# Kernel tuning notes

Measured on AMD Instinct MI355X. Metric: run time of the kernel, lower is better.

The kernel has to match this reference:

```python
import jax, jax.numpy as jnp
import numpy as np

N = 100000
E = 1600000
D_IN = 256
HID = 128
EPS = 1e-5


def setup_inputs() -> dict:
    key = jax.random.key(0)
    ks = jax.random.split(key, 8)
    x = jax.random.normal(ks[0], (N, D_IN), dtype=jnp.float32)
    edge_index = jax.random.randint(ks[1], (2, E), 0, N, dtype=jnp.int64)
    edge_weight = jax.random.uniform(ks[2], (E,), dtype=jnp.float32)
    # GCNConv lin weights (glorot-ish scale) + bias
    W1 = jax.random.normal(ks[3], (D_IN, HID), dtype=jnp.float32) / np.sqrt(D_IN)
    b1 = jnp.zeros((HID,), dtype=jnp.float32)
    W2 = jax.random.normal(ks[4], (HID, HID), dtype=jnp.float32) / np.sqrt(HID)
    b2 = jnp.zeros((HID,), dtype=jnp.float32)
    # BatchNorm affine params
    g1 = jnp.ones((HID,), dtype=jnp.float32)
    be1 = jnp.zeros((HID,), dtype=jnp.float32)
    g2 = jnp.ones((HID,), dtype=jnp.float32)
    be2 = jnp.zeros((HID,), dtype=jnp.float32)
    return {"x": x, "edge_index": edge_index, "edge_weight": edge_weight,
            "W1": W1, "b1": b1, "g1": g1, "be1": be1,
            "W2": W2, "b2": b2, "g2": g2, "be2": be2}


def _gcn_layer(h, src, dst, w, W, b):
    # GCNConv(add_self_loops=False, normalize=False):
    # h' = h @ W; out[i] = sum_{(j->i)} w_ji * h'[j]; out += b
    h = h @ W                                   # [N, out_dim]
    msg = w[:, None] * jnp.take(h, src, axis=0)  # [E, out_dim]
    agg = jax.ops.segment_sum(msg, dst, num_segments=N)
    return agg + b


def _bn(h, gamma, beta):
    # BatchNorm1d with batch statistics (biased variance), training-mode math
    mean = jnp.mean(h, axis=0)
    var = jnp.mean(jnp.square(h - mean), axis=0)
    return (h - mean) * jax.lax.rsqrt(var + EPS) * gamma + beta


def reference(x, edge_index, edge_weight, W1, b1, g1, be1, W2, b2, g2, be2):
    src = edge_index[0]
    dst = edge_index[1]
    h = _gcn_layer(x, src, dst, edge_weight, W1, b1)
    h = jax.nn.relu(_bn(h, g1, be1))
    h = _gcn_layer(h, src, dst, edge_weight, W2, b2)
    h = jax.nn.relu(_bn(h, g2, be2))  # last_activation=True
    return h
```

## Files before the change

### kernel.cpp

```cpp
#include <hip/hip_runtime.h>
#include <hip/hip_bf16.h>

#define NNODES 100000
#define DIN    256
#define NHID   128
#define EPS    1e-5f
#define SHIFT  9
#define NB2    ((NNODES + 511) >> SHIFT)
#define BCAP2  9216
#define CURPAD 16
#define PH     2048

typedef __attribute__((ext_vector_type(8))) short short8v;
typedef __attribute__((ext_vector_type(4))) float f32x4;

static __device__ __forceinline__ unsigned short f2bf(float v) {
    __hip_bfloat16 b = __float2bfloat16(v);
    return *reinterpret_cast<unsigned short*>(&b);
}
static __device__ __forceinline__ float bfhi2f(unsigned int u) {
    union { unsigned int i; float f; } x; x.i = u & 0xFFFF0000u; return x.f;
}
static __device__ __forceinline__ float bflo2f(unsigned int u) {
    union { unsigned int i; float f; } x; x.i = u << 16; return x.f;
}

__global__ __launch_bounds__(256) void prep_kernel(const float* __restrict__ W1,
                                                   const float* __restrict__ W2,
                                                   unsigned short* __restrict__ Wt1,
                                                   unsigned short* __restrict__ Wt2,
                                                   int* __restrict__ gcur,
                                                   float* __restrict__ sums) {
    int i = blockIdx.x * 256 + threadIdx.x;
    if (i < DIN * NHID) {
        const int k = i >> 7, c = i & 127;
        Wt1[c * DIN + k] = f2bf(W1[i]);
        return;
    }
    i -= DIN * NHID;
    if (i < NHID * NHID) {
        const int k = i >> 7, c = i & 127;
        Wt2[c * NHID + k] = f2bf(W2[i]);
        return;
    }
    i -= NHID * NHID;
    if (i < NB2 * CURPAD) { gcur[i] = 0; return; }
    i -= NB2 * CURPAD;
    if (i < 512) sums[i] = 0.f;
}

template <int K, int MODE>
__global__ __launch_bounds__(256) void mfma_gemm(const float* __restrict__ Af,
                                                 const unsigned short* __restrict__ Wtb,
                                                 const float* __restrict__ SS,
                                                 unsigned short* __restrict__ C, int M) {
    constexpr int NS = K / 32;
    constexpr int PADB = 40;
    __shared__ unsigned short As[2][64 * PADB];
    __shared__ float ssl[256];

    const int t = threadIdx.x;
    if (MODE == 1) {
        ssl[t] = SS[t];
        __syncthreads();
    }

    const int wid = t >> 6;
    const int lane = t & 63;
    const int wr = wid >> 1, wc = wid & 1;
    const int l15 = lane & 15, g = lane >> 4;
    const int R0 = blockIdx.x * 64;
    const int RW = R0 + wr * 32;

    const int srow = t >> 2;
    const int scol = (t & 3) * 8;

    f32x4 acc[2][4] = {};

    auto STAGE = [&](int s, int buf) {
        const int k0 = s * 32;
        int grow = R0 + srow;
        grow = grow < M ? grow : M - 1;
        const float* p = Af + (size_t)grow * K + k0 + scol;
        float4 v0 = *reinterpret_cast<const float4*>(p);
        float4 v1 = *reinterpret_cast<const float4*>(p + 4);
        if (MODE == 1) {
            const int c0 = k0 + scol;
            v0.x = fmaxf(fmaf(v0.x, ssl[c0],     ssl[128 + c0]),     0.f);
            v0.y = fmaxf(fmaf(v0.y, ssl[c0 + 1], ssl[128 + c0 + 1]), 0.f);
            v0.z = fmaxf(fmaf(v0.z, ssl[c0 + 2], ssl[128 + c0 + 2]), 0.f);
            v0.w = fmaxf(fmaf(v0.w, ssl[c0 + 3], ssl[128 + c0 + 3]), 0.f);
            v1.x = fmaxf(fmaf(v1.x, ssl[c0 + 4], ssl[128 + c0 + 4]), 0.f);
            v1.y = fmaxf(fmaf(v1.y, ssl[c0 + 5], ssl[128 + c0 + 5]), 0.f);
            v1.z = fmaxf(fmaf(v1.z, ssl[c0 + 6], ssl[128 + c0 + 6]), 0.f);
            v1.w = fmaxf(fmaf(v1.w, ssl[c0 + 7], ssl[128 + c0 + 7]), 0.f);
        }
        unsigned short bv[8];
        bv[0] = f2bf(v0.x); bv[1] = f2bf(v0.y); bv[2] = f2bf(v0.z); bv[3] = f2bf(v0.w);
        bv[4] = f2bf(v1.x); bv[5] = f2bf(v1.y); bv[6] = f2bf(v1.z); bv[7] = f2bf(v1.w);
        *reinterpret_cast<uint4*>(&As[buf][srow * PADB + scol]) =
            *reinterpret_cast<const uint4*>(bv);
    };

    STAGE(0, 0);
    __syncthreads();

    for (int s = 0; s < NS; ++s) {
        if (s + 1 < NS) STAGE(s + 1, (s + 1) & 1);
        const unsigned short* ab = As[s & 1];
        short8v b[4];
#pragma unroll
        for (int n = 0; n < 4; ++n) {
            const int col = wc * 64 + n * 16 + l15;
            b[n] = *reinterpret_cast<const short8v*>(&Wtb[(size_t)col * K + s * 32 + g * 8]);
        }
        short8v a[2];
#pragma unroll
        for (int m = 0; m < 2; ++m) {
            const int row = wr * 32 + m * 16 + l15;
            a[m] = *reinterpret_cast<const short8v*>(&ab[row * PADB + g * 8]);
        }
#pragma unroll
        for (int m = 0; m < 2; ++m)
#pragma unroll
            for (int n = 0; n < 4; ++n)
                acc[m][n] = __builtin_amdgcn_mfma_f32_16x16x32_bf16(a[m], b[n], acc[m][n], 0, 0, 0);
        __syncthreads();
    }

#pragma unroll
    for (int m = 0; m < 2; ++m) {
#pragma unroll
        for (int q = 0; q < 4; ++q) {
            const int row = RW + m * 16 + g * 4 + q;
            if (row < M) {
                unsigned short* cp = C + (size_t)row * NHID + wc * 64 + l15;
#pragma unroll
                for (int n = 0; n < 4; ++n)
                    cp[n * 16] = f2bf(acc[m][n][q]);
            }
        }
    }
}

__global__ __launch_bounds__(256) void part_kernel(const int* __restrict__ src,
                                                   const int* __restrict__ dst,
                                                   const float* __restrict__ w,
                                                   int* __restrict__ gcur,
                                                   int2* __restrict__ bstage, int E) {
    __shared__ int2 staged[PH];
    __shared__ unsigned char aux[PH];
    __shared__ int hist[NB2], scn[NB2], cur[NB2], gbase[NB2];
    __shared__ int part[256];

    const int t = threadIdx.x;
    const int nchunk = (E + PH - 1) / PH;
    for (int c = blockIdx.x; c < nchunk; c += gridDim.x) {
        const int e0 = c * PH;
        const int cnt = min(PH, E - e0);
        for (int i = t; i < NB2; i += 256) hist[i] = 0;
        __syncthreads();

        int2 pay[8];
        int bk[8];
#pragma unroll
        for (int j = 0; j < 8; ++j) {
            const int i = j * 256 + t;
            bk[j] = -1;
            if (i < cnt) {
                const int e = e0 + i;
                const int d = dst[e];
                bk[j] = d >> SHIFT;
                pay[j].x = src[e] | ((d & 511) << 17);
                pay[j].y = __float_as_int(w[e]);
                atomicAdd(&hist[bk[j]], 1);
            }
        }
        __syncthreads();

        part[t] = (t < NB2) ? hist[t] : 0;
        __syncthreads();
        for (int off = 1; off < 256; off <<= 1) {
            const int v = (t >= off) ? part[t - off] : 0;
            __syncthreads();
            part[t] += v;
            __syncthreads();
        }
        if (t < NB2) {
            const int ex = part[t] - hist[t];
            scn[t] = ex;
            cur[t] = ex;
        }
        __syncthreads();

#pragma unroll
        for (int j = 0; j < 8; ++j) {
            if (bk[j] >= 0) {
                const int p = atomicAdd(&cur[bk[j]], 1);
                staged[p] = pay[j];
                aux[p] = (unsigned char)bk[j];
            }
        }
        if (t < NB2 && hist[t] > 0) gbase[t] = atomicAdd(&gcur[t * CURPAD], hist[t]);
        __syncthreads();

        for (int i = t; i < cnt; i += 256) {
            const int b = aux[i];
            const int p = gbase[b] + (i - scn[b]);
            if (p < BCAP2) bstage[(size_t)b * BCAP2 + p] = staged[i];
        }
        __syncthreads();
    }
}

__global__ __launch_bounds__(512) void csr_kernel(const int* __restrict__ gcur,
                                                  const int2* __restrict__ bstage,
                                                  int2* __restrict__ row_be,
                                                  int2* __restrict__ s_iw) {
    const int b = blockIdx.x;
    const int t = threadIdx.x;
    int cnt = gcur[b * CURPAD];
    if (cnt > BCAP2) cnt = BCAP2;
    const int sbase = b * BCAP2;

    __shared__ int hist[512], cur[512];
    __shared__ int part[512];
    hist[t] = 0;
    __syncthreads();
    for (int i = t; i < cnt; i += 512)
        atomicAdd(&hist[(bstage[sbase + i].x >> 17) & 511], 1);
    __syncthreads();

    part[t] = hist[t];
    __syncthreads();
    for (int off = 1; off < 512; off <<= 1) {
        const int v = (t >= off) ? part[t - off] : 0;
        __syncthreads();
        part[t] += v;
        __syncthreads();
    }
    const int excl = part[t] - hist[t];
    cur[t] = excl;
    const int d = (b << SHIFT) + t;
    if (d < NNODES) {
        int2 be;
        be.x = sbase + excl;
        be.y = sbase + part[t];
        row_be[d] = be;
    }
    __syncthreads();

    for (int i = t; i < cnt; i += 512) {
        const int2 e = bstage[sbase + i];
        const int l = (e.x >> 17) & 511;
        const int p = atomicAdd(&cur[l], 1);
        int2 o;
        o.x = e.x & 0x1FFFF;
        o.y = e.y;
        s_iw[sbase + p] = o;
    }
}

__global__ __launch_bounds__(256) void aggregate_kernel(const unsigned short* __restrict__ hb,
                                                        const int2* __restrict__ row_be,
                                                        const int2* __restrict__ s_iw,
                                                        float* __restrict__ out, int n) {
    const int wid = (blockIdx.x * 256 + threadIdx.x) >> 6;
    if (wid >= n) return;
    const int lane = threadIdx.x & 63;
    const int grp = lane >> 4;
    const int l16 = lane & 15;
    const int2 be = row_be[wid];
    const int end = be.y;

    float acc[8] = {};
    int j = be.x + grp;
    for (; j + 4 < end; j += 8) {
        const int2 e0 = s_iw[j];
        const int2 e1 = s_iw[j + 4];
        const uint4 v0 = *reinterpret_cast<const uint4*>(hb + (size_t)e0.x * NHID + l16 * 8);
        const uint4 v1 = *reinterpret_cast<const uint4*>(hb + (size_t)e1.x * NHID + l16 * 8);
        const float w0 = __int_as_float(e0.y);
        const float w1 = __int_as_float(e1.y);
        acc[0] = fmaf(w0, bflo2f(v0.x), acc[0]); acc[1] = fmaf(w0, bfhi2f(v0.x), acc[1]);
        acc[2] = fmaf(w0, bflo2f(v0.y), acc[2]); acc[3] = fmaf(w0, bfhi2f(v0.y), acc[3]);
        acc[4] = fmaf(w0, bflo2f(v0.z), acc[4]); acc[5] = fmaf(w0, bfhi2f(v0.z), acc[5]);
        acc[6] = fmaf(w0, bflo2f(v0.w), acc[6]); acc[7] = fmaf(w0, bfhi2f(v0.w), acc[7]);
        acc[0] = fmaf(w1, bflo2f(v1.x), acc[0]); acc[1] = fmaf(w1, bfhi2f(v1.x), acc[1]);
        acc[2] = fmaf(w1, bflo2f(v1.y), acc[2]); acc[3] = fmaf(w1, bfhi2f(v1.y), acc[3]);
        acc[4] = fmaf(w1, bflo2f(v1.z), acc[4]); acc[5] = fmaf(w1, bfhi2f(v1.z), acc[5]);
        acc[6] = fmaf(w1, bflo2f(v1.w), acc[6]); acc[7] = fmaf(w1, bfhi2f(v1.w), acc[7]);
    }
    if (j < end) {
        const int2 e0 = s_iw[j];
        const uint4 v0 = *reinterpret_cast<const uint4*>(hb + (size_t)e0.x * NHID + l16 * 8);
        const float w0 = __int_as_float(e0.y);
        acc[0] = fmaf(w0, bflo2f(v0.x), acc[0]); acc[1] = fmaf(w0, bfhi2f(v0.x), acc[1]);
        acc[2] = fmaf(w0, bflo2f(v0.y), acc[2]); acc[3] = fmaf(w0, bfhi2f(v0.y), acc[3]);
        acc[4] = fmaf(w0, bflo2f(v0.z), acc[4]); acc[5] = fmaf(w0, bfhi2f(v0.z), acc[5]);
        acc[6] = fmaf(w0, bflo2f(v0.w), acc[6]); acc[7] = fmaf(w0, bfhi2f(v0.w), acc[7]);
    }
#pragma unroll
    for (int k = 0; k < 8; ++k) {
        acc[k] += __shfl_xor(acc[k], 16, 64);
        acc[k] += __shfl_xor(acc[k], 32, 64);
    }
    if (grp == 0) {
        float4 a, b;
        a.x = acc[0]; a.y = acc[1]; a.z = acc[2]; a.w = acc[3];
        b.x = acc[4]; b.y = acc[5]; b.z = acc[6]; b.w = acc[7];
        float4* op = reinterpret_cast<float4*>(out + (size_t)wid * NHID + l16 * 8);
        op[0] = a;
        op[1] = b;
    }
}

__global__ __launch_bounds__(256) void stats_kernel(const float* __restrict__ h,
                                                    float* __restrict__ sums, int nrows) {
    const int col = threadIdx.x & 127;
    const int half = threadIdx.x >> 7;
    float s = 0.f, sq = 0.f;
    for (int r = blockIdx.x * 2 + half; r < nrows; r += gridDim.x * 2) {
        const float v = h[(size_t)r * NHID + col];
        s += v;
        sq += v * v;
    }
    __shared__ float ls[256], lq[256];
    ls[threadIdx.x] = s;
    lq[threadIdx.x] = sq;
    __syncthreads();
    if (threadIdx.x < 128) {
        atomicAdd(&sums[col], ls[threadIdx.x] + ls[threadIdx.x + 128]);
        atomicAdd(&sums[128 + col], lq[threadIdx.x] + lq[threadIdx.x + 128]);
    }
}

__global__ void finalize_kernel(const float* __restrict__ sums,
                                const float* __restrict__ gamma,
                                const float* __restrict__ beta,
                                float* __restrict__ ss) {
    const int c = threadIdx.x;
    const float invN = 1.0f / (float)NNODES;
    const float mean = sums[c] * invN;
    const float var = sums[128 + c] * invN - mean * mean;
    const float scale = gamma[c] * rsqrtf(var + EPS);
    ss[c] = scale;
    ss[128 + c] = beta[c] - mean * scale;
}

__global__ __launch_bounds__(256) void apply_f32_kernel(const float* __restrict__ in,
                                                        const float* __restrict__ ss,
                                                        float* __restrict__ out, int n4) {
    const int idx = blockIdx.x * 256 + threadIdx.x;
    if (idx >= n4) return;
    const int c = (idx & 31) * 4;
    const float4 v = reinterpret_cast<const float4*>(in)[idx];
    const float4 sc = *reinterpret_cast<const float4*>(ss + c);
    const float4 sh = *reinterpret_cast<const float4*>(ss + 128 + c);
    float4 r;
    r.x = fmaxf(fmaf(v.x, sc.x, sh.x), 0.f);
    r.y = fmaxf(fmaf(v.y, sc.y, sh.y), 0.f);
    r.z = fmaxf(fmaf(v.z, sc.z, sh.z), 0.f);
    r.w = fmaxf(fmaf(v.w, sc.w, sh.w), 0.f);
    reinterpret_cast<float4*>(out)[idx] = r;
}

extern "C" void kernel_launch(void* const* d_in, const int* in_sizes, int n_in,
                              void* d_out, int out_size, void* d_ws, size_t ws_size,
                              hipStream_t stream) {
    const float* x   = (const float*)d_in[0];
    const int*   ei  = (const int*)d_in[1];
    const float* ew  = (const float*)d_in[2];
    const float* W1  = (const float*)d_in[3];
    const float* g1  = (const float*)d_in[5];
    const float* be1 = (const float*)d_in[6];
    const float* W2  = (const float*)d_in[7];
    const float* g2  = (const float*)d_in[9];
    const float* be2 = (const float*)d_in[10];
    float* out = (float*)d_out;

    const int M = NNODES;
    const int E = in_sizes[2];
    const int* src = ei;
    const int* dst = ei + E;

    unsigned short* hb = (unsigned short*)d_ws;
    float* agg   = (float*)(hb + (size_t)M * NHID);
    int2* bstage = (int2*)(agg + (size_t)M * NHID);
    int2* s_iw   = bstage + (size_t)NB2 * BCAP2;
    int2* row_be = s_iw + (size_t)NB2 * BCAP2;
    int* gcur    = (int*)(row_be + NNODES);
    unsigned short* Wt1b = (unsigned short*)(gcur + NB2 * CURPAD);
    unsigned short* Wt2b = Wt1b + DIN * NHID;
    float* sums  = (float*)(Wt2b + NHID * NHID);
    float* ss    = sums + 512;

    const int gemm_grid = (M + 63) / 64;
    const int n4 = M * NHID / 4;
    const int app_grid = (n4 + 255) / 256;
    const int agg_grid = (M * 64 + 255) / 256;
    const int part_grid = (E + PH - 1) / PH;
    const int prep_tot = DIN * NHID + NHID * NHID + NB2 * CURPAD + 512;

    prep_kernel<<<(prep_tot + 255) / 256, 256, 0, stream>>>(W1, W2, Wt1b, Wt2b, gcur, sums);
    part_kernel<<<part_grid, 256, 0, stream>>>(src, dst, ew, gcur, bstage, E);
    csr_kernel<<<NB2, 512, 0, stream>>>(gcur, bstage, row_be, s_iw);

    mfma_gemm<DIN, 0><<<gemm_grid, 256, 0, stream>>>(x, Wt1b, nullptr, hb, M);
    aggregate_kernel<<<agg_grid, 256, 0, stream>>>(hb, row_be, s_iw, agg, M);
    stats_kernel<<<1024, 256, 0, stream>>>(agg, sums, M);
    finalize_kernel<<<1, 128, 0, stream>>>(sums, g1, be1, ss);

    mfma_gemm<NHID, 1><<<gemm_grid, 256, 0, stream>>>(agg, Wt2b, ss, hb, M);
    aggregate_kernel<<<agg_grid, 256, 0, stream>>>(hb, row_be, s_iw, agg, M);
    stats_kernel<<<1024, 256, 0, stream>>>(agg, sums + 256, M);
    finalize_kernel<<<1, 128, 0, stream>>>(sums + 256, g2, be2, ss);
    apply_f32_kernel<<<app_grid, 256, 0, stream>>>(agg, ss, out, n4);
}
```

Before: 336.6 us.

## Fuse GEMM1 with edge partition, store aggregates in bf16, fold BN finalize

```diff
diff --git a/kernel.cpp b/kernel.cpp
--- a/kernel.cpp
+++ b/kernel.cpp
@@ -49,116 +49,96 @@
     if (i < 512) sums[i] = 0.f;
 }
 
-template <int K, int MODE>
-__global__ __launch_bounds__(256) void mfma_gemm(const float* __restrict__ Af,
-                                                 const unsigned short* __restrict__ Wtb,
-                                                 const float* __restrict__ SS,
-                                                 unsigned short* __restrict__ C, int M) {
-    constexpr int NS = K / 32;
-    constexpr int PADB = 40;
-    __shared__ unsigned short As[2][64 * PADB];
-    __shared__ float ssl[256];
+__global__ __launch_bounds__(256) void gemm1_part_kernel(
+    const float* __restrict__ Af, const unsigned short* __restrict__ Wtb,
+    unsigned short* __restrict__ C, int M, int ngemm,
+    const int* __restrict__ src, const int* __restrict__ dst,
+    const float* __restrict__ w, int* __restrict__ gcur,
+    int2* __restrict__ bstage, int E) {
+    struct GemmS { unsigned short As[2][64 * 40]; };
+    struct PartS {
+        int2 staged[PH];
+        int hist[NB2], scn[NB2], cur[NB2], gbase[NB2];
+        int pscan[256];
+        unsigned char aux[PH];
+    };
+    __shared__ union { GemmS g; PartS p; } sm;
 
     const int t = threadIdx.x;
-    if (MODE == 1) {
-        ssl[t] = SS[t];
-        __syncthreads();
-    }
-
-    const int wid = t >> 6;
-    const int lane = t & 63;
-    const int wr = wid >> 1, wc = wid & 1;
-    const int l15 = lane & 15, g = lane >> 4;
-    const int R0 = blockIdx.x * 64;
-    const int RW = R0 + wr * 32;
-
-    const int srow = t >> 2;
-    const int scol = (t & 3) * 8;
-
-    f32x4 acc[2][4] = {};
-
-    auto STAGE = [&](int s, int buf) {
-        const int k0 = s * 32;
-        int grow = R0 + srow;
-        grow = grow < M ? grow : M - 1;
-        const float* p = Af + (size_t)grow * K + k0 + scol;
-        float4 v0 = *reinterpret_cast<const float4*>(p);
-        float4 v1 = *reinterpret_cast<const float4*>(p + 4);
-        if (MODE == 1) {
-            const int c0 = k0 + scol;
-            v0.x = fmaxf(fmaf(v0.x, ssl[c0],     ssl[128 + c0]),     0.f);
-            v0.y = fmaxf(fmaf(v0.y, ssl[c0 + 1], ssl[128 + c0 + 1]), 0.f);
-            v0.z = fmaxf(fmaf(v0.z, ssl[c0 + 2], ssl[128 + c0 + 2]), 0.f);
-            v0.w = fmaxf(fmaf(v0.w, ssl[c0 + 3], ssl[128 + c0 + 3]), 0.f);
-            v1.x = fmaxf(fmaf(v1.x, ssl[c0 + 4], ssl[128 + c0 + 4]), 0.f);
-            v1.y = fmaxf(fmaf(v1.y, ssl[c0 + 5], ssl[128 + c0 + 5]), 0.f);
-            v1.z = fmaxf(fmaf(v1.z, ssl[c0 + 6], ssl[128 + c0 + 6]), 0.f);
-            v1.w = fmaxf(fmaf(v1.w, ssl[c0 + 7], ssl[128 + c0 + 7]), 0.f);
-        }
-        unsigned short bv[8];
-        bv[0] = f2bf(v0.x); bv[1] = f2bf(v0.y); bv[2] = f2bf(v0.z); bv[3] = f2bf(v0.w);
-        bv[4] = f2bf(v1.x); bv[5] = f2bf(v1.y); bv[6] = f2bf(v1.z); bv[7] = f2bf(v1.w);
-        *reinterpret_cast<uint4*>(&As[buf][srow * PADB + scol]) =
-            *reinterpret_cast<const uint4*>(bv);
-    };
-
-    STAGE(0, 0);
-    __syncthreads();
-
-    for (int s = 0; s < NS; ++s) {
-        if (s + 1 < NS) STAGE(s + 1, (s + 1) & 1);
-        const unsigned short* ab = As[s & 1];
-        short8v b[4];
-#pragma unroll
-        for (int n = 0; n < 4; ++n) {
-            const int col = wc * 64 + n * 16 + l15;
-            b[n] = *reinterpret_cast<const short8v*>(&Wtb[(size_t)col * K + s * 32 + g * 8]);
-        }
-        short8v a[2];
+    if (blockIdx.x < ngemm) {
+        constexpr int K = DIN;
+        constexpr int NS = K / 32;
+        constexpr int PADB = 40;
+        const int wid = t >> 6;
+        const int lane = t & 63;
+        const int wr = wid >> 1, wc = wid & 1;
+        const int l15 = lane & 15, g = lane >> 4;
+        const int R0 = blockIdx.x * 64;
+        const int RW = R0 + wr * 32;
+        const int srow = t >> 2;
+        const int scol = (t & 3) * 8;
+
+        f32x4 acc[2][4] = {};
+
+        auto STAGE = [&](int s, int buf) {
+            const int k0 = s * 32;
+            int grow = R0 + srow;
+            grow = grow < M ? grow : M - 1;
+            const float* p = Af + (size_t)grow * K + k0 + scol;
+            const float4 v0 = *reinterpret_cast<const float4*>(p);
+            const float4 v1 = *reinterpret_cast<const float4*>(p + 4);
+            unsigned short bv[8];
+            bv[0] = f2bf(v0.x); bv[1] = f2bf(v0.y); bv[2] = f2bf(v0.z); bv[3] = f2bf(v0.w);
+            bv[4] = f2bf(v1.x); bv[5] = f2bf(v1.y); bv[6] = f2bf(v1.z); bv[7] = f2bf(v1.w);
+            *reinterpret_cast<uint4*>(&sm.g.As[buf][srow * PADB + scol]) =
+                *reinterpret_cast<const uint4*>(bv);
+        };
+
+        STAGE(0, 0);
+        __syncthreads();
+
+        for (int s = 0; s < NS; ++s) {
+            if (s + 1 < NS) STAGE(s + 1, (s + 1) & 1);
+            const unsigned short* ab = sm.g.As[s & 1];
+            short8v b[4];
+#pragma unroll
+            for (int n = 0; n < 4; ++n) {
+                const int col = wc * 64 + n * 16 + l15;
+                b[n] = *reinterpret_cast<const short8v*>(&Wtb[(size_t)col * K + s * 32 + g * 8]);
+            }
+            short8v a[2];
+#pragma unroll
+            for (int m = 0; m < 2; ++m) {
+                const int row = wr * 32 + m * 16 + l15;
+                a[m] = *reinterpret_cast<const short8v*>(&ab[row * PADB + g * 8]);
+            }
+#pragma unroll
+            for (int m = 0; m < 2; ++m)
+#pragma unroll
+                for (int n = 0; n < 4; ++n)
+                    acc[m][n] = __builtin_amdgcn_mfma_f32_16x16x32_bf16(a[m], b[n], acc[m][n], 0, 0, 0);
+            __syncthreads();
+        }
+
 #pragma unroll
         for (int m = 0; m < 2; ++m) {
-            const int row = wr * 32 + m * 16 + l15;
-            a[m] = *reinterpret_cast<const short8v*>(&ab[row * PADB + g * 8]);
-        }
-#pragma unroll
-        for (int m = 0; m < 2; ++m)
-#pragma unroll
-            for (int n = 0; n < 4; ++n)
-                acc[m][n] = __builtin_amdgcn_mfma_f32_16x16x32_bf16(a[m], b[n], acc[m][n], 0, 0, 0);
-        __syncthreads();
-    }
-
-#pragma unroll
-    for (int m = 0; m < 2; ++m) {
-#pragma unroll
-        for (int q = 0; q < 4; ++q) {
-            const int row = RW + m * 16 + g * 4 + q;
-            if (row < M) {
-                unsigned short* cp = C + (size_t)row * NHID + wc * 64 + l15;
-#pragma unroll
-                for (int n = 0; n < 4; ++n)
-                    cp[n * 16] = f2bf(acc[m][n][q]);
-            }
-        }
-    }
-}
-
-__global__ __launch_bounds__(256) void part_kernel(const int* __restrict__ src,
-                                                   const int* __restrict__ dst,
-                                                   const float* __restrict__ w,
-                                                   int* __restrict__ gcur,
-                                                   int2* __restrict__ bstage, int E) {
-    __shared__ int2 staged[PH];
-    __shared__ unsigned char aux[PH];
-    __shared__ int hist[NB2], scn[NB2], cur[NB2], gbase[NB2];
-    __shared__ int part[256];
-
-    const int t = threadIdx.x;
-    const int nchunk = (E + PH - 1) / PH;
-    for (int c = blockIdx.x; c < nchunk; c += gridDim.x) {
+#pragma unroll
+            for (int q = 0; q < 4; ++q) {
+                const int row = RW + m * 16 + g * 4 + q;
+                if (row < M) {
+                    unsigned short* cp = C + (size_t)row * NHID + wc * 64 + l15;
+#pragma unroll
+                    for (int n = 0; n < 4; ++n)
+                        cp[n * 16] = f2bf(acc[m][n][q]);
+                }
+            }
+        }
+    } else {
+        const int c = blockIdx.x - ngemm;
         const int e0 = c * PH;
+        if (e0 >= E) return;
         const int cnt = min(PH, E - e0);
-        for (int i = t; i < NB2; i += 256) hist[i] = 0;
+        for (int i = t; i < NB2; i += 256) sm.p.hist[i] = 0;
         __syncthreads();
 
         int2 pay[8];
@@ -173,43 +153,43 @@
                 bk[j] = d >> SHIFT;
                 pay[j].x = src[e] | ((d & 511) << 17);
                 pay[j].y = __float_as_int(w[e]);
-                atomicAdd(&hist[bk[j]], 1);
-            }
-        }
-        __syncthreads();
-
-        part[t] = (t < NB2) ? hist[t] : 0;
+                atomicAdd(&sm.p.hist[bk[j]], 1);
+            }
+        }
+        __syncthreads();
+
+        sm.p.pscan[t] = (t < NB2) ? sm.p.hist[t] : 0;
         __syncthreads();
         for (int off = 1; off < 256; off <<= 1) {
-            const int v = (t >= off) ? part[t - off] : 0;
+            const int v = (t >= off) ? sm.p.pscan[t - off] : 0;
             __syncthreads();
-            part[t] += v;
+            sm.p.pscan[t] += v;
             __syncthreads();
         }
         if (t < NB2) {
-            const int ex = part[t] - hist[t];
-            scn[t] = ex;
-            cur[t] = ex;
+            const int ex = sm.p.pscan[t] - sm.p.hist[t];
+            sm.p.scn[t] = ex;
+            sm.p.cur[t] = ex;
         }
         __syncthreads();
 
 #pragma unroll
         for (int j = 0; j < 8; ++j) {
             if (bk[j] >= 0) {
-                const int p = atomicAdd(&cur[bk[j]], 1);
-                staged[p] = pay[j];
-                aux[p] = (unsigned char)bk[j];
-            }
-        }
-        if (t < NB2 && hist[t] > 0) gbase[t] = atomicAdd(&gcur[t * CURPAD], hist[t]);
+                const int p = atomicAdd(&sm.p.cur[bk[j]], 1);
+                sm.p.staged[p] = pay[j];
+                sm.p.aux[p] = (unsigned char)bk[j];
+            }
+        }
+        if (t < NB2 && sm.p.hist[t] > 0)
+            sm.p.gbase[t] = atomicAdd(&gcur[t * CURPAD], sm.p.hist[t]);
         __syncthreads();
 
         for (int i = t; i < cnt; i += 256) {
-            const int b = aux[i];
-            const int p = gbase[b] + (i - scn[b]);
-            if (p < BCAP2) bstage[(size_t)b * BCAP2 + p] = staged[i];
-        }
-        __syncthreads();
+            const int b = sm.p.aux[i];
+            const int p = sm.p.gbase[b] + (i - sm.p.scn[b]);
+            if (p < BCAP2) bstage[(size_t)b * BCAP2 + p] = sm.p.staged[i];
+        }
     }
 }
 
@@ -264,7 +244,7 @@
 __global__ __launch_bounds__(256) void aggregate_kernel(const unsigned short* __restrict__ hb,
                                                         const int2* __restrict__ row_be,
                                                         const int2* __restrict__ s_iw,
-                                                        float* __restrict__ out, int n) {
+                                                        unsigned short* __restrict__ outB, int n) {
     const int wid = (blockIdx.x * 256 + threadIdx.x) >> 6;
     if (wid >= n) return;
     const int lane = threadIdx.x & 63;
@@ -306,63 +286,162 @@
         acc[k] += __shfl_xor(acc[k], 32, 64);
     }
     if (grp == 0) {
-        float4 a, b;
-        a.x = acc[0]; a.y = acc[1]; a.z = acc[2]; a.w = acc[3];
-        b.x = acc[4]; b.y = acc[5]; b.z = acc[6]; b.w = acc[7];
-        float4* op = reinterpret_cast<float4*>(out + (size_t)wid * NHID + l16 * 8);
-        op[0] = a;
-        op[1] = b;
-    }
-}
-
-__global__ __launch_bounds__(256) void stats_kernel(const float* __restrict__ h,
+        unsigned short bv[8];
+#pragma unroll
+        for (int k = 0; k < 8; ++k) bv[k] = f2bf(acc[k]);
+        *reinterpret_cast<uint4*>(outB + (size_t)wid * NHID + l16 * 8) =
+            *reinterpret_cast<const uint4*>(bv);
+    }
+}
+
+__global__ __launch_bounds__(256) void stats_kernel(const unsigned short* __restrict__ h,
                                                     float* __restrict__ sums, int nrows) {
-    const int col = threadIdx.x & 127;
-    const int half = threadIdx.x >> 7;
-    float s = 0.f, sq = 0.f;
-    for (int r = blockIdx.x * 2 + half; r < nrows; r += gridDim.x * 2) {
-        const float v = h[(size_t)r * NHID + col];
-        s += v;
-        sq += v * v;
-    }
-    __shared__ float ls[256], lq[256];
-    ls[threadIdx.x] = s;
-    lq[threadIdx.x] = sq;
-    __syncthreads();
-    if (threadIdx.x < 128) {
-        atomicAdd(&sums[col], ls[threadIdx.x] + ls[threadIdx.x + 128]);
-        atomicAdd(&sums[128 + col], lq[threadIdx.x] + lq[threadIdx.x + 128]);
-    }
-}
-
-__global__ void finalize_kernel(const float* __restrict__ sums,
-                                const float* __restrict__ gamma,
-                                const float* __restrict__ beta,
-                                float* __restrict__ ss) {
-    const int c = threadIdx.x;
-    const float invN = 1.0f / (float)NNODES;
-    const float mean = sums[c] * invN;
-    const float var = sums[128 + c] * invN - mean * mean;
-    const float scale = gamma[c] * rsqrtf(var + EPS);
-    ss[c] = scale;
-    ss[128 + c] = beta[c] - mean * scale;
-}
-
-__global__ __launch_bounds__(256) void apply_f32_kernel(const float* __restrict__ in,
-                                                        const float* __restrict__ ss,
-                                                        float* __restrict__ out, int n4) {
-    const int idx = blockIdx.x * 256 + threadIdx.x;
-    if (idx >= n4) return;
-    const int c = (idx & 31) * 4;
-    const float4 v = reinterpret_cast<const float4*>(in)[idx];
-    const float4 sc = *reinterpret_cast<const float4*>(ss + c);
-    const float4 sh = *reinterpret_cast<const float4*>(ss + 128 + c);
-    float4 r;
-    r.x = fmaxf(fmaf(v.x, sc.x, sh.x), 0.f);
-    r.y = fmaxf(fmaf(v.y, sc.y, sh.y), 0.f);
-    r.z = fmaxf(fmaf(v.z, sc.z, sh.z), 0.f);
-    r.w = fmaxf(fmaf(v.w, sc.w, sh.w), 0.f);
-    reinterpret_cast<float4*>(out)[idx] = r;
+    const int t = threadIdx.x;
+    const int cp = t & 63;
+    const int rg = t >> 6;
+    float s0 = 0.f, s1 = 0.f, q0 = 0.f, q1 = 0.f;
+    for (int r = blockIdx.x * 4 + rg; r < nrows; r += gridDim.x * 4) {
+        const unsigned int v = *reinterpret_cast<const unsigned int*>(h + (size_t)r * NHID + cp * 2);
+        const float a = bflo2f(v), b = bfhi2f(v);
+        s0 += a; q0 = fmaf(a, a, q0);
+        s1 += b; q1 = fmaf(b, b, q1);
+    }
+    __shared__ float ls[4][128], lq[4][128];
+    ls[rg][cp * 2] = s0; ls[rg][cp * 2 + 1] = s1;
+    lq[rg][cp * 2] = q0; lq[rg][cp * 2 + 1] = q1;
+    __syncthreads();
+    if (t < 128) {
+        atomicAdd(&sums[t], ls[0][t] + ls[1][t] + ls[2][t] + ls[3][t]);
+    } else {
+        const int c = t - 128;
+        atomicAdd(&sums[128 + c], lq[0][c] + lq[1][c] + lq[2][c] + lq[3][c]);
+    }
+}
+
+__global__ __launch_bounds__(256) void mfma_gemm2(const unsigned short* __restrict__ Ab,
+                                                  const unsigned short* __restrict__ Wtb,
+                                                  const float* __restrict__ sums,
+                                                  const float* __restrict__ gamma,
+                                                  const float* __restrict__ beta,
+                                                  unsigned short* __restrict__ C, int M) {
+    constexpr int K = NHID;
+    constexpr int NS = K / 32;
+    constexpr int PADB = 40;
+    __shared__ unsigned short As[2][64 * PADB];
+    __shared__ float ssl[256];
+
+    const int t = threadIdx.x;
+    if (t < 128) {
+        const float invN = 1.0f / (float)NNODES;
+        const float mean = sums[t] * invN;
+        const float var = sums[128 + t] * invN - mean * mean;
+        const float scale = gamma[t] * rsqrtf(var + EPS);
+        ssl[t] = scale;
+        ssl[128 + t] = beta[t] - mean * scale;
+    }
+    __syncthreads();
+
+    const int wid = t >> 6;
+    const int lane = t & 63;
+    const int wr = wid >> 1, wc = wid & 1;
+    const int l15 = lane & 15, g = lane >> 4;
+    const int R0 = blockIdx.x * 64;
+    const int RW = R0 + wr * 32;
+    const int srow = t >> 2;
+    const int scol = (t & 3) * 8;
+
+    f32x4 acc[2][4] = {};
+
+    auto STAGE = [&](int s, int buf) {
+        const int k0 = s * 32;
+        int grow = R0 + srow;
+        grow = grow < M ? grow : M - 1;
+        const uint4 v = *reinterpret_cast<const uint4*>(Ab + (size_t)grow * K + k0 + scol);
+        const float f[8] = {bflo2f(v.x), bfhi2f(v.x), bflo2f(v.y), bfhi2f(v.y),
+                            bflo2f(v.z), bfhi2f(v.z), bflo2f(v.w), bfhi2f(v.w)};
+        const int c0 = k0 + scol;
+        unsigned short bv[8];
+#pragma unroll
+        for (int j = 0; j < 8; ++j)
+            bv[j] = f2bf(fmaxf(fmaf(f[j], ssl[c0 + j], ssl[128 + c0 + j]), 0.f));
+        *reinterpret_cast<uint4*>(&As[buf][srow * PADB + scol]) =
+            *reinterpret_cast<const uint4*>(bv);
+    };
+
+    STAGE(0, 0);
+    __syncthreads();
+
+    for (int s = 0; s < NS; ++s) {
+        if (s + 1 < NS) STAGE(s + 1, (s + 1) & 1);
+        const unsigned short* ab = As[s & 1];
+        short8v b[4];
+#pragma unroll
+        for (int n = 0; n < 4; ++n) {
+            const int col = wc * 64 + n * 16 + l15;
+            b[n] = *reinterpret_cast<const short8v*>(&Wtb[(size_t)col * K + s * 32 + g * 8]);
+        }
+        short8v a[2];
+#pragma unroll
+        for (int m = 0; m < 2; ++m) {
+            const int row = wr * 32 + m * 16 + l15;
+            a[m] = *reinterpret_cast<const short8v*>(&ab[row * PADB + g * 8]);
+        }
+#pragma unroll
+        for (int m = 0; m < 2; ++m)
+#pragma unroll
+            for (int n = 0; n < 4; ++n)
+                acc[m][n] = __builtin_amdgcn_mfma_f32_16x16x32_bf16(a[m], b[n], acc[m][n], 0, 0, 0);
+        __syncthreads();
+    }
+
+#pragma unroll
+    for (int m = 0; m < 2; ++m) {
+#pragma unroll
+        for (int q = 0; q < 4; ++q) {
+            const int row = RW + m * 16 + g * 4 + q;
+            if (row < M) {
+                unsigned short* cp = C + (size_t)row * NHID + wc * 64 + l15;
+#pragma unroll
+                for (int n = 0; n < 4; ++n)
+                    cp[n * 16] = f2bf(acc[m][n][q]);
+            }
+        }
+    }
+}
+
+__global__ __launch_bounds__(256) void apply_kernel(const unsigned short* __restrict__ aggB,
+                                                    const float* __restrict__ sums,
+                                                    const float* __restrict__ gamma,
+                                                    const float* __restrict__ beta,
+                                                    float* __restrict__ out, int n8) {
+    __shared__ float ss[256];
+    const int t = threadIdx.x;
+    if (t < 128) {
+        const float invN = 1.0f / (float)NNODES;
+        const float mean = sums[t] * invN;
+        const float var = sums[128 + t] * invN - mean * mean;
+        const float scale = gamma[t] * rsqrtf(var + EPS);
+        ss[t] = scale;
+        ss[128 + t] = beta[t] - mean * scale;
+    }
+    __syncthreads();
+    const int idx = blockIdx.x * 256 + t;
+    if (idx >= n8) return;
+    const int c0 = (idx & 15) * 8;
+    const uint4 v = reinterpret_cast<const uint4*>(aggB)[idx];
+    const float f[8] = {bflo2f(v.x), bfhi2f(v.x), bflo2f(v.y), bfhi2f(v.y),
+                        bflo2f(v.z), bfhi2f(v.z), bflo2f(v.w), bfhi2f(v.w)};
+    float4 r0, r1;
+    r0.x = fmaxf(fmaf(f[0], ss[c0],     ss[128 + c0]),     0.f);
+    r0.y = fmaxf(fmaf(f[1], ss[c0 + 1], ss[128 + c0 + 1]), 0.f);
+    r0.z = fmaxf(fmaf(f[2], ss[c0 + 2], ss[128 + c0 + 2]), 0.f);
+    r0.w = fmaxf(fmaf(f[3], ss[c0 + 3], ss[128 + c0 + 3]), 0.f);
+    r1.x = fmaxf(fmaf(f[4], ss[c0 + 4], ss[128 + c0 + 4]), 0.f);
+    r1.y = fmaxf(fmaf(f[5], ss[c0 + 5], ss[128 + c0 + 5]), 0.f);
+    r1.z = fmaxf(fmaf(f[6], ss[c0 + 6], ss[128 + c0 + 6]), 0.f);
+    r1.w = fmaxf(fmaf(f[7], ss[c0 + 7], ss[128 + c0 + 7]), 0.f);
+    reinterpret_cast<float4*>(out)[idx * 2] = r0;
+    reinterpret_cast<float4*>(out)[idx * 2 + 1] = r1;
 }
 
 extern "C" void kernel_launch(void* const* d_in, const int* in_sizes, int n_in,
@@ -384,36 +463,33 @@
     const int* src = ei;
     const int* dst = ei + E;
 
-    unsigned short* hb = (unsigned short*)d_ws;
-    float* agg   = (float*)(hb + (size_t)M * NHID);
-    int2* bstage = (int2*)(agg + (size_t)M * NHID);
+    unsigned short* hb   = (unsigned short*)d_ws;
+    unsigned short* aggB = hb + (size_t)M * NHID;
+    int2* bstage = (int2*)(aggB + (size_t)M * NHID);
     int2* s_iw   = bstage + (size_t)NB2 * BCAP2;
     int2* row_be = s_iw + (size_t)NB2 * BCAP2;
     int* gcur    = (int*)(row_be + NNODES);
     unsigned short* Wt1b = (unsigned short*)(gcur + NB2 * CURPAD);
     unsigned short* Wt2b = Wt1b + DIN * NHID;
     float* sums  = (float*)(Wt2b + NHID * NHID);
-    float* ss    = sums + 512;
 
     const int gemm_grid = (M + 63) / 64;
-    const int n4 = M * NHID / 4;
-    const int app_grid = (n4 + 255) / 256;
+    const int n8 = M * NHID / 8;
+    const int app_grid = (n8 + 255) / 256;
     const int agg_grid = (M * 64 + 255) / 256;
     const int part_grid = (E + PH - 1) / PH;
     const int prep_tot = DIN * NHID + NHID * NHID + NB2 * CURPAD + 512;
 
     prep_kernel<<<(prep_tot + 255) / 256, 256, 0, stream>>>(W1, W2, Wt1b, Wt2b, gcur, sums);
-    part_kernel<<<part_grid, 256, 0, stream>>>(src, dst, ew, gcur, bstage, E);
+    gemm1_part_kernel<<<gemm_grid + part_grid, 256, 0, stream>>>(
+        x, Wt1b, hb, M, gemm_grid, src, dst, ew, gcur, bstage, E);
     csr_kernel<<<NB2, 512, 0, stream>>>(gcur, bstage, row_be, s_iw);
 
-    mfma_gemm<DIN, 0><<<gemm_grid, 256, 0, stream>>>(x, Wt1b, nullptr, hb, M);
-    aggregate_kernel<<<agg_grid, 256, 0, stream>>>(hb, row_be, s_iw, agg, M);
-    stats_kernel<<<1024, 256, 0, stream>>>(agg, sums, M);
-    finalize_kernel<<<1, 128, 0, stream>>>(sums, g1, be1, ss);
-
-    mfma_gemm<NHID, 1><<<gemm_grid, 256, 0, stream>>>(agg, Wt2b, ss, hb, M);
-    aggregate_kernel<<<agg_grid, 256, 0, stream>>>(hb, row_be, s_iw, agg, M);
-    stats_kernel<<<1024, 256, 0, stream>>>(agg, sums + 256, M);
-    finalize_kernel<<<1, 128, 0, stream>>>(sums + 256, g2, be2, ss);
-    apply_f32_kernel<<<app_grid, 256, 0, stream>>>(agg, ss, out, n4);
-}
+    aggregate_kernel<<<agg_grid, 256, 0, stream>>>(hb, row_be, s_iw, aggB, M);
+    stats_kernel<<<1024, 256, 0, stream>>>(aggB, sums, M);
+
+    mfma_gemm2<<<gemm_grid, 256, 0, stream>>>(aggB, Wt2b, sums, g1, be1, hb, M);
+    aggregate_kernel<<<agg_grid, 256, 0, stream>>>(hb, row_be, s_iw, aggB, M);
+    stats_kernel<<<1024, 256, 0, stream>>>(aggB, sums + 256, M);
+    apply_kernel<<<app_grid, 256, 0, stream>>>(aggB, sums + 256, g2, be2, out, n8);
+}
```

After: 293.9 us, median of 2. 1.15x faster.
